# Kernel optimization log

Measured on AMD Instinct MI355X. Metric: run time of the kernel, lower is better.

The kernel has to match this reference:

```python
import jax, jax.numpy as jnp
import numpy as np


def setup_inputs() -> dict:
    key = jax.random.key(0)
    k_x, k_w1, k_w2, k_w3 = jax.random.split(key, 4)
    input_dim, hidden_dim, num_classes = 4096, 4096, 1000
    batch = 8192
    x = jax.random.normal(k_x, (batch, input_dim), dtype=jnp.float32)
    # BinaryLinear params: weight ~ N(0,1)*0.1, bias zeros
    w1 = jax.random.normal(k_w1, (hidden_dim, input_dim), dtype=jnp.float32) * 0.1
    b1 = jnp.zeros((hidden_dim,), dtype=jnp.float32)
    w2 = jax.random.normal(k_w2, (hidden_dim, hidden_dim), dtype=jnp.float32) * 0.1
    b2 = jnp.zeros((hidden_dim,), dtype=jnp.float32)
    # fc3: plain nn.Linear (kaiming-uniform-ish; any init works for a numerics baseline)
    bound = 1.0 / np.sqrt(hidden_dim)
    w3 = jax.random.uniform(k_w3, (num_classes, hidden_dim), dtype=jnp.float32, minval=-bound, maxval=bound)
    b3 = jnp.zeros((num_classes,), dtype=jnp.float32)
    return {"x": x, "w1": w1, "b1": b1, "w2": w2, "b2": b2, "w3": w3, "b3": b3}


def _binary_linear(x, w, b):
    # sign-binarize both activations and weights, then fp32 GEMM + bias
    return jnp.sign(x) @ jnp.sign(w).T + b


def reference(x, w1, b1, w2, b2, w3, b3):
    h1 = _binary_linear(x, w1, b1)          # [B, H]
    a1 = jnp.sign(h1)
    h2 = _binary_linear(a1, w2, b2)         # [B, H]
    a2 = jnp.sign(h2)
    out = a2 @ w3.T + b3                    # [B, C] plain fp32 linear
    return out
```

## Files before the change

kernel.cpp:

```cpp
#include <hip/hip_runtime.h>
#include <hip/hip_bf16.h>


typedef __attribute__((ext_vector_type(4))) float f32x4;
typedef __attribute__((ext_vector_type(4))) int   i32x4;
typedef __attribute__((ext_vector_type(8))) int   i32x8;

#define BM 128
#define BN 128

__device__ __forceinline__ void async_copy16(const void* g, void* l) {
  __builtin_amdgcn_global_load_lds(
      (const __attribute__((address_space(1))) void*)g,
      (__attribute__((address_space(3))) void*)l,
      16, 0, 0);
}

__device__ __forceinline__ char sign8(float v) {
  return (v > 0.f) ? (char)1 : ((v < 0.f) ? (char)-1 : (char)0);
}
__device__ __forceinline__ unsigned nib4(float v) {
  return (v > 0.f) ? 0x2u : ((v < 0.f) ? 0xAu : 0x0u);
}

__global__ void sign_pack_fp4_3(const float* __restrict__ x,
                                const float* __restrict__ w1,
                                const float* __restrict__ w2,
                                unsigned* __restrict__ out,
                                int n8x, int n8w) {
  int i = blockIdx.x * blockDim.x + threadIdx.x;
  if (i >= n8x + 2 * n8w) return;
  const float* in;
  int k;
  if (i < n8x)            { in = x;  k = i; }
  else if (i < n8x + n8w) { in = w1; k = i - n8x; }
  else                    { in = w2; k = i - n8x - n8w; }
  const float4* p = (const float4*)in + (size_t)k * 2;
  float4 v0 = p[0], v1 = p[1];
  unsigned b0 = nib4(v0.x) | (nib4(v0.y) << 4);
  unsigned b1 = nib4(v0.z) | (nib4(v0.w) << 4);
  unsigned b2 = nib4(v1.x) | (nib4(v1.y) << 4);
  unsigned b3 = nib4(v1.z) | (nib4(v1.w) << 4);
  out[i] = b0 | (b1 << 8) | (b2 << 16) | (b3 << 24);
}

__global__ __launch_bounds__(256)
void w3_quant(const float* __restrict__ in, char* __restrict__ out,
              float* __restrict__ scale, int rows_valid) {
  const int row = blockIdx.x;
  const int tid = threadIdx.x;
  int* orow = (int*)(out + (size_t)row * 4096);
  if (row >= rows_valid) {
#pragma unroll
    for (int j = 0; j < 4; ++j) orow[j * 256 + tid] = 0;
    if (tid == 0) scale[row] = 0.f;
    return;
  }
  const float4* p = (const float4*)(in + (size_t)row * 4096);
  float4 v[4];
  float amax = 0.f;
#pragma unroll
  for (int j = 0; j < 4; ++j) {
    v[j] = p[j * 256 + tid];
    amax = fmaxf(amax, fmaxf(fmaxf(fabsf(v[j].x), fabsf(v[j].y)),
                             fmaxf(fabsf(v[j].z), fabsf(v[j].w))));
  }
#pragma unroll
  for (int m = 32; m >= 1; m >>= 1)
    amax = fmaxf(amax, __shfl_xor(amax, m, 64));
  __shared__ float wmax[4];
  if ((tid & 63) == 0) wmax[tid >> 6] = amax;
  __syncthreads();
  const float rowmax = fmaxf(fmaxf(wmax[0], wmax[1]), fmaxf(wmax[2], wmax[3]));
  const float inv = (rowmax > 0.f) ? 127.f / rowmax : 0.f;
#pragma unroll
  for (int j = 0; j < 4; ++j) {
    int q0 = (int)rintf(v[j].x * inv);
    int q1 = (int)rintf(v[j].y * inv);
    int q2 = (int)rintf(v[j].z * inv);
    int q3 = (int)rintf(v[j].w * inv);
    unsigned r = ((unsigned)(unsigned char)(char)q0)
               | ((unsigned)(unsigned char)(char)q1 << 8)
               | ((unsigned)(unsigned char)(char)q2 << 16)
               | ((unsigned)(unsigned char)(char)q3 << 24);
    orow[j * 256 + tid] = (int)r;
  }
  if (tid == 0) scale[row] = rowmax * (1.f / 127.f);
}


__device__ __forceinline__ void fp4_compute(const unsigned char* Asb,
                                            const unsigned char* Bsb,
                                            int wy, int wx, int fr, int swz,
                                            f32x4 (&acc)[4][4]) {
  i32x8 a[4], b[4];
#pragma unroll
  for (int i = 0; i < 4; ++i) {
    i32x4 t = *(const i32x4*)(Asb + (wy * 64 + i * 16 + fr) * 64 + swz);
    a[i] = (i32x8){t[0], t[1], t[2], t[3], 0, 0, 0, 0};
  }
#pragma unroll
  for (int j = 0; j < 4; ++j) {
    i32x4 t = *(const i32x4*)(Bsb + (wx * 64 + j * 16 + fr) * 64 + swz);
    b[j] = (i32x8){t[0], t[1], t[2], t[3], 0, 0, 0, 0};
  }
#pragma unroll
  for (int i = 0; i < 4; ++i)
#pragma unroll
    for (int j = 0; j < 4; ++j)
      acc[i][j] = __builtin_amdgcn_mfma_scale_f32_16x16x128_f8f6f4(
          a[i], b[j], acc[i][j],
          4, 4,
          0, 0x7f7f7f7f,
          0, 0x7f7f7f7f);
}

__device__ __forceinline__ void i8_compute(const char* Asb, const char* Bsb,
                                           int wy, int wx, int fr, int swz,
                                           i32x4 (&acc)[4][4]) {
  i32x4 a[4], b[4];
#pragma unroll
  for (int i = 0; i < 4; ++i)
    a[i] = *(const i32x4*)(Asb + (wy * 64 + i * 16 + fr) * 64 + swz);
#pragma unroll
  for (int j = 0; j < 4; ++j)
    b[j] = *(const i32x4*)(Bsb + (wx * 64 + j * 16 + fr) * 64 + swz);
#pragma unroll
  for (int i = 0; i < 4; ++i)
#pragma unroll
    for (int j = 0; j < 4; ++j)
      acc[i][j] = __builtin_amdgcn_mfma_i32_16x16x64_i8(a[i], b[j], acc[i][j], 0, 0, 0);
}

template <int EPI>
__global__ __launch_bounds__(256)
void gemm_fp4(const unsigned char* __restrict__ A,
              const unsigned char* __restrict__ B,
              const float* __restrict__ bias,
              unsigned* __restrict__ Cp4,
              char* __restrict__ Ci8,
              int Kb, int ldc)
{
  __shared__ unsigned char As0[128 * 64];
  __shared__ unsigned char As1[128 * 64];
  __shared__ unsigned char Bs0[128 * 64];
  __shared__ unsigned char Bs1[128 * 64];

  const int tid  = threadIdx.x;
  const int lane = tid & 63;
  const int wid  = tid >> 6;
  const int wy   = wid >> 1;
  const int wx   = wid & 1;

  const int m0 = blockIdx.y * BM;
  const int n0 = blockIdx.x * BN;

  const int r1 = tid >> 2;
  const int r2 = r1 + 64;
  const int c1 = (tid & 3) ^ ((r1 >> 1) & 3);
  const int c2 = (tid & 3) ^ ((r2 >> 1) & 3);
  const unsigned char* Ag1 = A + (size_t)(m0 + r1) * Kb + c1 * 16;
  const unsigned char* Ag2 = A + (size_t)(m0 + r2) * Kb + c2 * 16;
  const unsigned char* Bg1 = B + (size_t)(n0 + r1) * Kb + c1 * 16;
  const unsigned char* Bg2 = B + (size_t)(n0 + r2) * Kb + c2 * 16;
  const int sl1 = tid * 16;
  const int sl2 = (tid + 256) * 16;

  f32x4 acc[4][4];
#pragma unroll
  for (int i = 0; i < 4; ++i)
#pragma unroll
    for (int j = 0; j < 4; ++j)
      acc[i][j] = (f32x4){0.f, 0.f, 0.f, 0.f};

  const int fr  = lane & 15;
  const int kc  = lane >> 4;
  const int swz = (kc ^ ((fr >> 1) & 3)) * 16;

  for (int k0 = 0; k0 < Kb; k0 += 128) {
    async_copy16(Ag1 + k0,      As0 + sl1);
    async_copy16(Ag1 + k0 + 64, As1 + sl1);
    async_copy16(Ag2 + k0,      As0 + sl2);
    async_copy16(Ag2 + k0 + 64, As1 + sl2);
    async_copy16(Bg1 + k0,      Bs0 + sl1);
    async_copy16(Bg1 + k0 + 64, Bs1 + sl1);
    async_copy16(Bg2 + k0,      Bs0 + sl2);
    async_copy16(Bg2 + k0 + 64, Bs1 + sl2);
    __syncthreads();

    fp4_compute(As0, Bs0, wy, wx, fr, swz, acc);
    fp4_compute(As1, Bs1, wy, wx, fr, swz, acc);
    __syncthreads();
  }

  const int ccol = lane & 15;
  const int crow = (lane >> 4) * 4;

  if (EPI == 1) {
#pragma unroll
    for (int i = 0; i < 4; ++i) {
      const int m = m0 + wy * 64 + i * 16 + crow;
#pragma unroll
      for (int j = 0; j < 4; ++j) {
        const int n = n0 + wx * 64 + j * 16 + ccol;
        const float bv = bias[n];
#pragma unroll
        for (int r = 0; r < 4; ++r)
          Ci8[(size_t)(m + r) * ldc + n] = sign8(acc[i][j][r] + bv);
      }
    }
  } else {
#pragma unroll
    for (int i = 0; i < 4; ++i) {
      const int m = m0 + wy * 64 + i * 16 + crow;
#pragma unroll
      for (int r = 0; r < 4; ++r) {
        unsigned w32[4];
#pragma unroll
        for (int j = 0; j < 4; ++j) {
          const int n = n0 + wx * 64 + j * 16 + ccol;
          unsigned nb = nib4(acc[i][j][r] + bias[n]);
          unsigned pb = nb | (((unsigned)__shfl_xor((int)nb, 1)) << 4);
          unsigned w  = pb | (((unsigned)__shfl_xor((int)pb, 2)) << 8);
          w32[j]      = w  | (((unsigned)__shfl_xor((int)w,  4)) << 16);
        }
        if ((ccol & 7) == 0) {
          const size_t rowb = (size_t)(m + r) * (ldc >> 3);
#pragma unroll
          for (int j = 0; j < 4; ++j)
            Cp4[rowb + ((n0 + wx * 64 + j * 16 + ccol) >> 3)] = w32[j];
        }
      }
    }
  }
}

__global__ __launch_bounds__(256)
void gemm_i8(const char* __restrict__ A,
             const char* __restrict__ B,
             const float* __restrict__ scale,
             const float* __restrict__ bias,
             float* __restrict__ Cf,
             int Kb, int ldc, int nvalid)
{
  __shared__ char As0[128 * 64];
  __shared__ char As1[128 * 64];
  __shared__ char Bs0[128 * 64];
  __shared__ char Bs1[128 * 64];

  const int tid  = threadIdx.x;
  const int lane = tid & 63;
  const int wid  = tid >> 6;
  const int wy   = wid >> 1;
  const int wx   = wid & 1;

  const int m0 = blockIdx.y * BM;
  const int n0 = blockIdx.x * BN;

  const int r1 = tid >> 2;
  const int r2 = r1 + 64;
  const int c1 = (tid & 3) ^ ((r1 >> 1) & 3);
  const int c2 = (tid & 3) ^ ((r2 >> 1) & 3);
  const char* Ag1 = A + (size_t)(m0 + r1) * Kb + c1 * 16;
  const char* Ag2 = A + (size_t)(m0 + r2) * Kb + c2 * 16;
  const char* Bg1 = B + (size_t)(n0 + r1) * Kb + c1 * 16;
  const char* Bg2 = B + (size_t)(n0 + r2) * Kb + c2 * 16;
  const int sl1 = tid * 16;
  const int sl2 = (tid + 256) * 16;

  i32x4 acc[4][4];
#pragma unroll
  for (int i = 0; i < 4; ++i)
#pragma unroll
    for (int j = 0; j < 4; ++j)
      acc[i][j] = (i32x4){0, 0, 0, 0};

  const int fr  = lane & 15;
  const int kc  = lane >> 4;
  const int swz = (kc ^ ((fr >> 1) & 3)) * 16;

  for (int k0 = 0; k0 < Kb; k0 += 128) {
    async_copy16(Ag1 + k0,      As0 + sl1);
    async_copy16(Ag1 + k0 + 64, As1 + sl1);
    async_copy16(Ag2 + k0,      As0 + sl2);
    async_copy16(Ag2 + k0 + 64, As1 + sl2);
    async_copy16(Bg1 + k0,      Bs0 + sl1);
    async_copy16(Bg1 + k0 + 64, Bs1 + sl1);
    async_copy16(Bg2 + k0,      Bs0 + sl2);
    async_copy16(Bg2 + k0 + 64, Bs1 + sl2);
    __syncthreads();

    i8_compute(As0, Bs0, wy, wx, fr, swz, acc);
    i8_compute(As1, Bs1, wy, wx, fr, swz, acc);
    __syncthreads();
  }

  const int ccol = lane & 15;
  const int crow = (lane >> 4) * 4;
#pragma unroll
  for (int i = 0; i < 4; ++i) {
    const int m = m0 + wy * 64 + i * 16 + crow;
#pragma unroll
    for (int j = 0; j < 4; ++j) {
      const int n = n0 + wx * 64 + j * 16 + ccol;
      if (n >= nvalid) continue;
      const float sv = scale[n];
      const float bv = bias[n];
#pragma unroll
      for (int r = 0; r < 4; ++r)
        Cf[(size_t)(m + r) * ldc + n] = (float)acc[i][j][r] * sv + bv;
    }
  }
}

extern "C" void kernel_launch(void* const* d_in, const int* in_sizes, int n_in,
                              void* d_out, int out_size, void* d_ws, size_t ws_size,
                              hipStream_t stream) {
  const float* x  = (const float*)d_in[0];
  const float* w1 = (const float*)d_in[1];
  const float* b1 = (const float*)d_in[2];
  const float* w2 = (const float*)d_in[3];
  const float* b2 = (const float*)d_in[4];
  const float* w3 = (const float*)d_in[5];
  const float* b3 = (const float*)d_in[6];

  const int Mb = 8192, H = 4096, C = 1000, Cpad = 1024;
  const int Kb = H / 2;

  char* ws = (char*)d_ws;
  unsigned* xp  = (unsigned*)(ws);
  char*     w3q = ws + (size_t)33554432;
  float*    s3  = (float*)(ws + (size_t)37748736);
  unsigned* a1p = (unsigned*)(ws + (size_t)41943040);
  char*     a2  = ws + (size_t)58720256;
  unsigned* w1p = (unsigned*)(ws + (size_t)16777216);
  unsigned* w2p = (unsigned*)(ws + (size_t)25165824);

  const int n8x = Mb * H / 8;
  const int n8w = H * H / 8;
  sign_pack_fp4_3<<<(n8x + 2 * n8w + 255) / 256, 256, 0, stream>>>(
      x, w1, w2, xp, n8x, n8w);
  w3_quant<<<Cpad, 256, 0, stream>>>(w3, w3q, s3, C);

  dim3 blk(256);
  gemm_fp4<0><<<dim3(H / BN, Mb / BM), blk, 0, stream>>>(
      (const unsigned char*)xp, (const unsigned char*)w1p, b1, a1p, nullptr, Kb, H);
  gemm_fp4<1><<<dim3(H / BN, Mb / BM), blk, 0, stream>>>(
      (const unsigned char*)a1p, (const unsigned char*)w2p, b2, nullptr, a2, Kb, H);
  gemm_i8<<<dim3(Cpad / BN, Mb / BM), blk, 0, stream>>>(
      a2, w3q, s3, b3, (float*)d_out, H, C, C);
}
```

Before: 517.8 us.

## Double-buffer LDS tiles to overlap async global loads with MFMA compute

Both GEMM kernels now use a two-stage LDS ping-pong with 64-wide K steps. The next tile's async global-to-LDS copies are issued before computing the current tile, and there is one barrier per iteration instead of two. The aim is to hide global load latency behind MFMA work. In exchange each iteration covers half as much K, so there are more loop trips and barriers overall, and the overlap relies on the async copy completing before the barrier.

```diff
diff --git a/kernel.cpp b/kernel.cpp
--- a/kernel.cpp
+++ b/kernel.cpp
@@ -141,10 +141,8 @@
               char* __restrict__ Ci8,
               int Kb, int ldc)
 {
-  __shared__ unsigned char As0[128 * 64];
-  __shared__ unsigned char As1[128 * 64];
-  __shared__ unsigned char Bs0[128 * 64];
-  __shared__ unsigned char Bs1[128 * 64];
+  __shared__ unsigned char As[2][128 * 64];
+  __shared__ unsigned char Bs[2][128 * 64];
 
   const int tid  = threadIdx.x;
   const int lane = tid & 63;
@@ -177,21 +175,25 @@
   const int kc  = lane >> 4;
   const int swz = (kc ^ ((fr >> 1) & 3)) * 16;
 
-  for (int k0 = 0; k0 < Kb; k0 += 128) {
-    async_copy16(Ag1 + k0,      As0 + sl1);
-    async_copy16(Ag1 + k0 + 64, As1 + sl1);
-    async_copy16(Ag2 + k0,      As0 + sl2);
-    async_copy16(Ag2 + k0 + 64, As1 + sl2);
-    async_copy16(Bg1 + k0,      Bs0 + sl1);
-    async_copy16(Bg1 + k0 + 64, Bs1 + sl1);
-    async_copy16(Bg2 + k0,      Bs0 + sl2);
-    async_copy16(Bg2 + k0 + 64, Bs1 + sl2);
+#define STAGE_FP4(buf, k0)                                   \
+  do {                                                       \
+    async_copy16(Ag1 + (k0), As[buf] + sl1);                 \
+    async_copy16(Ag2 + (k0), As[buf] + sl2);                 \
+    async_copy16(Bg1 + (k0), Bs[buf] + sl1);                 \
+    async_copy16(Bg2 + (k0), Bs[buf] + sl2);                 \
+  } while (0)
+
+  const int NIT = Kb >> 6;
+  STAGE_FP4(0, 0);
+  __syncthreads();
+
+#pragma unroll 1
+  for (int it = 0; it < NIT; ++it) {
+    if (it + 1 < NIT) STAGE_FP4((it + 1) & 1, (it + 1) * 64);
+    fp4_compute(As[it & 1], Bs[it & 1], wy, wx, fr, swz, acc);
     __syncthreads();
-
-    fp4_compute(As0, Bs0, wy, wx, fr, swz, acc);
-    fp4_compute(As1, Bs1, wy, wx, fr, swz, acc);
-    __syncthreads();
-  }
+  }
+#undef STAGE_FP4
 
   const int ccol = lane & 15;
   const int crow = (lane >> 4) * 4;
@@ -243,10 +245,8 @@
              float* __restrict__ Cf,
              int Kb, int ldc, int nvalid)
 {
-  __shared__ char As0[128 * 64];
-  __shared__ char As1[128 * 64];
-  __shared__ char Bs0[128 * 64];
-  __shared__ char Bs1[128 * 64];
+  __shared__ char As[2][128 * 64];
+  __shared__ char Bs[2][128 * 64];
 
   const int tid  = threadIdx.x;
   const int lane = tid & 63;
@@ -279,21 +279,25 @@
   const int kc  = lane >> 4;
   const int swz = (kc ^ ((fr >> 1) & 3)) * 16;
 
-  for (int k0 = 0; k0 < Kb; k0 += 128) {
-    async_copy16(Ag1 + k0,      As0 + sl1);
-    async_copy16(Ag1 + k0 + 64, As1 + sl1);
-    async_copy16(Ag2 + k0,      As0 + sl2);
-    async_copy16(Ag2 + k0 + 64, As1 + sl2);
-    async_copy16(Bg1 + k0,      Bs0 + sl1);
-    async_copy16(Bg1 + k0 + 64, Bs1 + sl1);
-    async_copy16(Bg2 + k0,      Bs0 + sl2);
-    async_copy16(Bg2 + k0 + 64, Bs1 + sl2);
+#define STAGE_I8(buf, k0)                                    \
+  do {                                                       \
+    async_copy16(Ag1 + (k0), As[buf] + sl1);                 \
+    async_copy16(Ag2 + (k0), As[buf] + sl2);                 \
+    async_copy16(Bg1 + (k0), Bs[buf] + sl1);                 \
+    async_copy16(Bg2 + (k0), Bs[buf] + sl2);                 \
+  } while (0)
+
+  const int NIT = Kb >> 6;
+  STAGE_I8(0, 0);
+  __syncthreads();
+
+#pragma unroll 1
+  for (int it = 0; it < NIT; ++it) {
+    if (it + 1 < NIT) STAGE_I8((it + 1) & 1, (it + 1) * 64);
+    i8_compute(As[it & 1], Bs[it & 1], wy, wx, fr, swz, acc);
     __syncthreads();
-
-    i8_compute(As0, Bs0, wy, wx, fr, swz, acc);
-    i8_compute(As1, Bs1, wy, wx, fr, swz, acc);
-    __syncthreads();
-  }
+  }
+#undef STAGE_I8
 
   const int ccol = lane & 15;
   const int crow = (lane >> 4) * 4;
```

After: 530.0 us. +2.3%, slower.
